# Optimization experiments

Measured on AMD Instinct MI355X. Metric: run time of the kernel, lower is better.

The kernel has to match this reference:

```python
import jax, jax.numpy as jnp
import numpy as np

HEADS = 8
EPS = 1e-6

def _feature_map(x):
    return jax.nn.elu(x) + 1.0

def _linear_attention(q, k, v, motion_weight):
    # q,k,v: [..., N, dh]; motion_weight broadcastable to q or None
    q = _feature_map(q)
    k = _feature_map(k)
    if motion_weight is not None:
        q = q * motion_weight
    k_sum = k.sum(axis=-2, keepdims=True)                      # [...,1,dh]
    kv = jnp.einsum('...nd,...ne->...de', k, v)                # [...,dh,dh]
    out = jnp.einsum('...nd,...de->...ne', q, kv)              # [...,N,dh]
    z = 1.0 / (jnp.einsum('...nd,...md->...nm', q, k_sum) + EPS)  # [...,N,1]
    return out * z

def setup_inputs() -> dict:
    key = jax.random.key(0)
    k1, k2, k3, k4 = jax.random.split(key, 4)
    B, T, H, W, C = 2, 16, 48, 48, 512
    x = jax.random.normal(k1, (B, T, H, W, C), dtype=jnp.float32)
    motion_mag = jax.random.normal(k2, (B, T, H, W, 1), dtype=jnp.float32)
    W_qkv = jax.random.normal(k3, (C, 3 * C), dtype=jnp.float32) * 0.02
    temporal_emb = jax.random.normal(k4, (1, 1, 1, 1, C), dtype=jnp.float32)
    return {"x": x, "motion_mag": motion_mag, "W_qkv": W_qkv, "temporal_emb": temporal_emb}

def _split_heads(t, lead, n, heads, dh):
    # t: [lead, n, heads*dh] -> [lead, heads, n, dh]
    return t.reshape(lead, n, heads, dh).transpose(0, 2, 1, 3)

def reference(x, motion_mag, W_qkv, temporal_emb):
    B, T, H, W, C = x.shape
    dh = C // HEADS
    x = x + temporal_emb

    # ---- temporal linear attention over frame-averaged tokens ----
    x_time = x.reshape(B, T, H * W, C).mean(axis=2)            # [B,T,C]
    qkv = x_time @ W_qkv                                       # [B,T,3C]
    q, k, v = jnp.split(qkv, 3, axis=-1)
    q = _split_heads(q, B, T, HEADS, dh)                       # [B,h,T,dh]
    k = _split_heads(k, B, T, HEADS, dh)
    v = _split_heads(v, B, T, HEADS, dh)
    mm = motion_mag.reshape(B, T, -1).mean(axis=-1, keepdims=True)  # [B,T,1]
    mw_t = 1.0 + jnp.tanh(mm)[:, None]                         # [B,1,T,1]
    t_out = _linear_attention(q, k, v, mw_t)                   # [B,h,T,dh]
    t_out = t_out.transpose(0, 2, 1, 3).reshape(B, T, C)       # [B,T,C]

    # broadcast temporal output over spatial dims
    x_sp = x + t_out[:, :, None, None, :]                      # [B,T,H,W,C]

    # ---- global spatial linear attention per frame ----
    N = H * W
    x_flat = x_sp.reshape(B * T, N, C)
    qkv = x_flat @ W_qkv                                       # [BT,N,3C]
    q, k, v = jnp.split(qkv, 3, axis=-1)
    q = _split_heads(q, B * T, N, HEADS, dh)                   # [BT,h,N,dh]
    k = _split_heads(k, B * T, N, HEADS, dh)
    v = _split_heads(v, B * T, N, HEADS, dh)
    mm2 = motion_mag.reshape(B * T, N, 1)
    mw_s = 1.0 + jnp.tanh(mm2)[:, None]                        # [BT,1,N,1]
    s_out = _linear_attention(q, k, v, mw_s)                   # [BT,h,N,dh]
    s_out = s_out.transpose(0, 2, 1, 3).reshape(B, T, H, W, C)
    return s_out
```

## Files before the change

kernel.cpp:

```cpp
#include <hip/hip_runtime.h>
#include <cstddef>
#include <cstdint>

#define HEADS 8
#define DH 64
#define C 512
#define TC 1536
#define BT 32
#define NTOK 2304
#define TT 16
#define EPS 1e-6f

typedef __attribute__((ext_vector_type(8))) short bf16x8;
typedef __attribute__((ext_vector_type(4))) float f32x4;
typedef __attribute__((address_space(3))) void as3_void;
typedef __attribute__((address_space(1))) const void as1_cvoid;

__device__ __forceinline__ float fmap(float x) {
    return x > 0.f ? x + 1.f : __expf(x);
}
__device__ __forceinline__ unsigned short f2bf(float f) {
    unsigned int u = __float_as_uint(f);
    return (unsigned short)((u + 0x7fffu + ((u >> 16) & 1u)) >> 16);
}
__device__ __forceinline__ unsigned int pack2bf(float a, float b) {
    return (unsigned int)f2bf(a) | ((unsigned int)f2bf(b) << 16);
}
__device__ __forceinline__ float bf2f(unsigned short h) {
    return __uint_as_float(((unsigned int)h) << 16);
}
__device__ __forceinline__ void gload16(const void* g, void* l) {
    __builtin_amdgcn_global_load_lds((as1_cvoid*)(uintptr_t)g,
                                     (as3_void*)(uintptr_t)l, 16, 0, 0);
}

__global__ __launch_bounds__(256) void k_prep_w(
    const float* __restrict__ W, unsigned short* __restrict__ Wt) {
    __shared__ float tile[32][33];
    int col0 = blockIdx.x * 32, c0 = blockIdx.y * 32;
    int tx = threadIdx.x & 31, ty = threadIdx.x >> 5;
#pragma unroll
    for (int j = 0; j < 4; ++j) {
        int c = ty + j * 8;
        tile[c][tx] = W[(size_t)(c0 + c) * TC + col0 + tx];
    }
    __syncthreads();
#pragma unroll
    for (int j = 0; j < 4; ++j) {
        int col = ty + j * 8;
        Wt[(size_t)(col0 + col) * C + c0 + tx] = f2bf(tile[tx][col]);
    }
}

__global__ __launch_bounds__(256) void k_time_reduce(
    const float* __restrict__ x, const float* __restrict__ motion,
    float* __restrict__ xtraw, float* __restrict__ mmraw,
    unsigned short* __restrict__ xb) {
    int bt = blockIdx.x, sp = blockIdx.y, tid = threadIdx.x;
    int n0 = sp * 288, cid = tid * 2;
    const float* xp = x + ((size_t)(bt * NTOK + n0)) * C + cid;
    unsigned short* xbp = xb + ((size_t)(bt * NTOK + n0)) * C + cid;
    float s0 = 0.f, s1 = 0.f;
    for (int n = 0; n < 288; ++n) {
        float2 v = *(const float2*)(xp + (size_t)n * C);
        s0 += v.x;
        s1 += v.y;
        *(unsigned int*)(xbp + (size_t)n * C) = pack2bf(v.x, v.y);
    }
    atomicAdd(&xtraw[bt * C + cid], s0);
    atomicAdd(&xtraw[bt * C + cid + 1], s1);

    const float* mp = motion + (size_t)bt * NTOK + n0;
    float m = mp[tid];
    if (tid < 32) m += mp[256 + tid];
    __shared__ float red[256];
    red[tid] = m;
    __syncthreads();
    for (int s = 128; s > 0; s >>= 1) {
        if (tid < s) red[tid] += red[tid + s];
        __syncthreads();
    }
    if (tid == 0) atomicAdd(&mmraw[bt], red[0]);
}

__global__ __launch_bounds__(256) void k_time_qkv(
    const float* __restrict__ xtraw, const float* __restrict__ temb,
    const float* __restrict__ W, float* __restrict__ qkvt) {
    int bt = blockIdx.x, col = blockIdx.y * 256 + threadIdx.x, tid = threadIdx.x;
    __shared__ float xl[C];
    xl[tid]       = xtraw[bt * C + tid]       * (1.f / NTOK) + temb[tid];
    xl[tid + 256] = xtraw[bt * C + tid + 256] * (1.f / NTOK) + temb[tid + 256];
    __syncthreads();
    float a = 0.f;
#pragma unroll 8
    for (int c = 0; c < C; ++c) a += xl[c] * W[(size_t)c * TC + col];
    qkvt[(size_t)bt * TC + col] = a;
}

__global__ __launch_bounds__(256) void k_time_attn(
    const float* __restrict__ qkvt, const float* __restrict__ mmraw,
    const float* __restrict__ temb, float* __restrict__ bias) {
    int b = blockIdx.x, h = blockIdx.y, tid = threadIdx.x;
    int d = tid & 63, g = tid >> 6;
    __shared__ float qs[TT][DH], ks[TT][DH], vs[TT][DH], ksum[DH];
    __shared__ float kvl[DH][DH];
    for (int t = g; t < TT; t += 4) {
        size_t base = (size_t)(b * TT + t) * TC + h * DH + d;
        float mwt = 1.f + tanhf(mmraw[b * TT + t] * (1.f / NTOK));
        qs[t][d] = fmap(qkvt[base]) * mwt;
        ks[t][d] = fmap(qkvt[base + C]);
        vs[t][d] = qkvt[base + 2 * C];
    }
    __syncthreads();
    if (g == 0) {
        float s = 0.f;
        for (int t = 0; t < TT; ++t) s += ks[t][d];
        ksum[d] = s;
    }
    float kva[16];
#pragma unroll
    for (int i = 0; i < 16; ++i) kva[i] = 0.f;
    for (int t = 0; t < TT; ++t) {
        float kd = ks[t][d];
#pragma unroll
        for (int i = 0; i < 16; ++i) kva[i] += kd * vs[t][g * 16 + i];
    }
#pragma unroll
    for (int i = 0; i < 16; ++i) kvl[d][g * 16 + i] = kva[i];
    __syncthreads();
    for (int tt = 0; tt < 4; ++tt) {
        int t = g * 4 + tt;
        float acc = 0.f, zden = 0.f;
        for (int dd = 0; dd < DH; ++dd) {
            float qv = qs[t][dd];
            acc  += qv * kvl[dd][d];
            zden += qv * ksum[dd];
        }
        bias[(size_t)(b * TT + t) * C + h * DH + d] =
            acc / (zden + EPS) + temb[h * DH + d];
    }
}

__global__ __launch_bounds__(256) void k_bias_vec(
    const float* __restrict__ bias, const float* __restrict__ W,
    float* __restrict__ bvec) {
    int bt = blockIdx.x, col = blockIdx.y * 256 + threadIdx.x, tid = threadIdx.x;
    __shared__ float bl[C];
    bl[tid]       = bias[bt * C + tid];
    bl[tid + 256] = bias[bt * C + tid + 256];
    __syncthreads();
    float a = 0.f;
#pragma unroll 8
    for (int c = 0; c < C; ++c) a += bl[c] * W[(size_t)c * TC + col];
    bvec[(size_t)bt * TC + col] = a;
}

__global__ __launch_bounds__(512) void k_spatial_kv(
    const unsigned short* __restrict__ xb, const unsigned short* __restrict__ Wt,
    const float* __restrict__ bvec, float* __restrict__ kvw,
    float* __restrict__ ksw) {
    __shared__ __align__(16) char smem[99328];
    unsigned short* A0 = (unsigned short*)smem;
    unsigned short* B0 = (unsigned short*)(smem + 16384);
    unsigned short* A1 = (unsigned short*)(smem + 49152);
    unsigned short* B1 = (unsigned short*)(smem + 65536);
    char* kvT = smem + 16384;
    float* bvl = (float*)(smem + 98304);

    const int s = blockIdx.x, hp = blockIdx.y, bt = blockIdx.z;
    const int tid = threadIdx.x, lane = tid & 63, w = tid >> 6;
    const int lm = lane & 15, quad = lane >> 4;
    const int mr = w & 1, nc = w >> 1;
    const int li8 = lane >> 3, lp = lane & 7;

    if (tid < 256) {
        int h2 = tid >> 7, j2 = tid & 127;
        int wr = (j2 < 64) ? (C + (hp * 2 + h2) * DH + j2)
                           : (2 * C + (hp * 2 + h2) * DH + (j2 - 64));
        bvl[tid] = bvec[(size_t)bt * TC + wr];
    }
    const unsigned short* srcA[2];
#pragma unroll
    for (int l = 0; l < 2; ++l) {
        int row = w * 16 + l * 8 + li8;
        int c = lp ^ (row & 7);
        srcA[l] = xb + ((size_t)(bt * NTOK + row)) * C + c * 8;
    }
    const unsigned short* srcB[4];
#pragma unroll
    for (int l = 0; l < 4; ++l) {
        int r = w * 32 + l * 8 + li8;
        int c = lp ^ (r & 7);
        int h2 = r >> 7, j2 = r & 127;
        int wr = (j2 < 64) ? (C + (hp * 2 + h2) * DH + j2)
                           : (2 * C + (hp * 2 + h2) * DH + (j2 - 64));
        srcB[l] = Wt + (size_t)wr * C + c * 8;
    }

    float ksp0 = 0.f, ksp1 = 0.f;
    f32x4 kvacc[2][2];
#pragma unroll
    for (int a = 0; a < 2; ++a)
#pragma unroll
        for (int b = 0; b < 2; ++b) kvacc[a][b] = (f32x4)0.f;

    auto STAGE = [&](unsigned short* As, unsigned short* Bs, int n0, int kc) {
#pragma unroll
        for (int l = 0; l < 2; ++l)
            gload16(srcA[l] + (size_t)n0 * C + kc * 64, As + (w * 16 + l * 8) * 64);
#pragma unroll
        for (int l = 0; l < 4; ++l)
            gload16(srcB[l] + kc * 64, Bs + (w * 32 + l * 8) * 64);
    };

#pragma unroll 1
    for (int t = 0; t < 3; ++t) {
        const int n0 = (s * 3 + t) * 128;
        f32x4 acc[4][4];
#pragma unroll
        for (int i = 0; i < 4; ++i)
#pragma unroll
            for (int j = 0; j < 4; ++j) acc[i][j] = (f32x4)0.f;

        STAGE(A0, B0, n0, 0);
        __syncthreads();
#pragma unroll
        for (int kc = 0; kc < 8; ++kc) {
            const unsigned short* As = (kc & 1) ? A1 : A0;
            const unsigned short* Bs = (kc & 1) ? B1 : B0;
            if (kc < 7) {
                STAGE((kc & 1) ? A0 : A1, (kc & 1) ? B0 : B1, n0, kc + 1);
                __builtin_amdgcn_sched_barrier(0);
            }
#pragma unroll
            for (int ks = 0; ks < 2; ++ks) {
                bf16x8 af[4], bfr[4];
#pragma unroll
                for (int i = 0; i < 4; ++i) {
                    int row = mr * 64 + i * 16 + lm;
                    int p = (ks * 4 + quad) ^ (row & 7);
                    af[i] = *(const bf16x8*)&As[row * 64 + p * 8];
                }
#pragma unroll
                for (int j = 0; j < 4; ++j) {
                    int row = nc * 64 + j * 16 + lm;
                    int p = (ks * 4 + quad) ^ (row & 7);
                    bfr[j] = *(const bf16x8*)&Bs[row * 64 + p * 8];
                }
#pragma unroll
                for (int i = 0; i < 4; ++i)
#pragma unroll
                    for (int j = 0; j < 4; ++j)
                        acc[i][j] = __builtin_amdgcn_mfma_f32_16x16x32_bf16(
                            af[i], bfr[j], acc[i][j], 0, 0, 0);
            }
            __syncthreads();
        }
#pragma unroll 1
        for (int ph = 0; ph < 2; ++ph) {
            __syncthreads();
            if ((nc >> 1) == ph) {
#pragma unroll
                for (int i = 0; i < 4; ++i) {
                    int tokb = mr * 64 + i * 16 + quad * 4;
                    int tc = tokb >> 3;
#pragma unroll
                    for (int j = 0; j < 4; ++j) {
                        int cg = nc * 64 + j * 16 + lm;
                        int cl = cg & 127;
                        float bv = bvl[cg];
                        f32x4 a4 = acc[i][j];
                        float v0 = a4[0] + bv, v1 = a4[1] + bv;
                        float v2 = a4[2] + bv, v3 = a4[3] + bv;
                        if (cl < 64) {
                            v0 = fmap(v0); v1 = fmap(v1);
                            v2 = fmap(v2); v3 = fmap(v3);
                        }
                        int p = (tc & 8) | ((tc & 7) ^ (cl & 7));
                        uint2 pk;
                        pk.x = pack2bf(v0, v1);
                        pk.y = pack2bf(v2, v3);
                        *(uint2*)(kvT + cl * 256 + p * 16 + (tokb & 7) * 2) = pk;
                    }
                }
            }
            __syncthreads();
            if (tid < 128) {
                int d = tid & 63, half = tid >> 6;
                float ssum = 0.f;
#pragma unroll
                for (int tc2 = 0; tc2 < 8; ++tc2) {
                    int tcc = half * 8 + tc2;
                    int p = (tcc & 8) | ((tcc & 7) ^ (d & 7));
                    bf16x8 v8 = *(const bf16x8*)(kvT + d * 256 + p * 16);
#pragma unroll
                    for (int q = 0; q < 8; ++q)
                        ssum += bf2f((unsigned short)v8[q]);
                }
                if (ph == 0) ksp0 += ssum; else ksp1 += ssum;
            }
#pragma unroll
            for (int dt2 = 0; dt2 < 2; ++dt2) {
                int drow = (mr * 2 + dt2) * 16 + lm;
                int erow = 64 + nc * 16 + lm;
#pragma unroll
                for (int ks2 = 0; ks2 < 4; ++ks2) {
                    int tcc = ks2 * 4 + quad;
                    int pA = (tcc & 8) | ((tcc & 7) ^ (drow & 7));
                    int pB = (tcc & 8) | ((tcc & 7) ^ (erow & 7));
                    bf16x8 ak = *(const bf16x8*)(kvT + drow * 256 + pA * 16);
                    bf16x8 bv8 = *(const bf16x8*)(kvT + erow * 256 + pB * 16);
                    kvacc[ph][dt2] = __builtin_amdgcn_mfma_f32_16x16x32_bf16(
                        ak, bv8, kvacc[ph][dt2], 0, 0, 0);
                }
            }
        }
        __syncthreads();
    }
#pragma unroll
    for (int ph = 0; ph < 2; ++ph) {
        float* kvp = kvw + (size_t)(bt * HEADS + hp * 2 + ph) * DH * DH;
#pragma unroll
        for (int dt2 = 0; dt2 < 2; ++dt2) {
            int d0 = (mr * 2 + dt2) * 16 + quad * 4;
            int e = nc * 16 + lm;
#pragma unroll
            for (int r = 0; r < 4; ++r)
                atomicAdd(&kvp[(d0 + r) * DH + e], kvacc[ph][dt2][r]);
        }
    }
    if (tid < 128) {
        int d = tid & 63;
        atomicAdd(&ksw[(bt * HEADS + hp * 2 + 0) * DH + d], ksp0);
        atomicAdd(&ksw[(bt * HEADS + hp * 2 + 1) * DH + d], ksp1);
    }
}

__global__ __launch_bounds__(256) void k_spatial_out(
    const unsigned short* __restrict__ xb, const unsigned short* __restrict__ Wt,
    const float* __restrict__ bvec, const float* __restrict__ motion,
    const float* __restrict__ kvw, const float* __restrict__ ksw,
    float* __restrict__ out) {
    __shared__ __align__(16) char smem[51712];
    unsigned short* A_s = (unsigned short*)smem;
    unsigned short* B_s = (unsigned short*)(smem + 16384);
    char* qs  = smem;
    char* kvT = smem + 32768;
    float* bvl = (float*)(smem + 49152);
    float* mwv = (float*)(smem + 49664);
    float* ksl = (float*)(smem + 50176);
    float* zv  = (float*)(smem + 50688);

    const int tile = blockIdx.x, hp = blockIdx.y, bt = blockIdx.z;
    const int tid = threadIdx.x, lane = tid & 63, w = tid >> 6;
    const int lm = lane & 15, quad = lane >> 4;
    const int mr = w & 1, nc = w >> 1;
    const int li8 = lane >> 3, lp = lane & 7;
    const int n0 = tile * 128;

    if (tid < 128) {
        bvl[tid] = bvec[(size_t)bt * TC + hp * 128 + tid];
        mwv[tid] = 1.f + tanhf(motion[(size_t)bt * NTOK + n0 + tid]);
        ksl[tid] = ksw[(bt * HEADS + hp * 2 + (tid >> 6)) * DH + (tid & 63)];
    }
    {
        int rr = tid & 127, hh = tid >> 7;
        int head = rr >> 6, e = rr & 63;
        const float* kvp = kvw + (size_t)(bt * HEADS + hp * 2 + head) * DH * DH;
#pragma unroll 8
        for (int d = hh * 32; d < hh * 32 + 32; ++d) {
            int p = (d >> 3) ^ (rr & 7);
            ((unsigned short*)(kvT + rr * 128 + p * 16))[d & 7] = f2bf(kvp[d * DH + e]);
        }
    }
    f32x4 acc[4][4];
#pragma unroll
    for (int i = 0; i < 4; ++i)
#pragma unroll
        for (int j = 0; j < 4; ++j) acc[i][j] = (f32x4)0.f;

    for (int kc = 0; kc < 8; ++kc) {
        __syncthreads();
#pragma unroll
        for (int l = 0; l < 4; ++l) {
            int rowbase = w * 32 + l * 8;
            int row = rowbase + li8;
            int c = lp ^ (row & 7);
            gload16(xb + ((size_t)(bt * NTOK + n0 + row)) * C + kc * 64 + c * 8,
                    A_s + rowbase * 64);
        }
#pragma unroll
        for (int l = 0; l < 4; ++l) {
            int rowbase = w * 32 + l * 8;
            int r = rowbase + li8;
            int c = lp ^ (r & 7);
            gload16(Wt + (size_t)(hp * 128 + r) * C + kc * 64 + c * 8,
                    B_s + rowbase * 64);
        }
        __syncthreads();
#pragma unroll
        for (int ks = 0; ks < 2; ++ks) {
            bf16x8 af[4], bfr[4];
#pragma unroll
            for (int i = 0; i < 4; ++i) {
                int row = mr * 64 + i * 16 + lm;
                int p = (ks * 4 + quad) ^ (row & 7);
                af[i] = *(const bf16x8*)&A_s[row * 64 + p * 8];
            }
#pragma unroll
            for (int j = 0; j < 4; ++j) {
                int row = nc * 64 + j * 16 + lm;
                int p = (ks * 4 + quad) ^ (row & 7);
                bfr[j] = *(const bf16x8*)&B_s[row * 64 + p * 8];
            }
#pragma unroll
            for (int i = 0; i < 4; ++i)
#pragma unroll
                for (int j = 0; j < 4; ++j)
                    acc[i][j] = __builtin_amdgcn_mfma_f32_16x16x32_bf16(
                        af[i], bfr[j], acc[i][j], 0, 0, 0);
        }
    }
    __syncthreads();
#pragma unroll
    for (int i = 0; i < 4; ++i) {
#pragma unroll
        for (int j = 0; j < 4; ++j) {
            int cl = nc * 64 + j * 16 + lm;
            float bv = bvl[cl];
            int cch = cl >> 3;
#pragma unroll
            for (int r = 0; r < 4; ++r) {
                int tok = mr * 64 + i * 16 + quad * 4 + r;
                float qv = fmap(acc[i][j][r] + bv) * mwv[tok];
                int p = (cch & 8) | ((cch & 7) ^ (tok & 7));
                ((unsigned short*)(qs + tok * 256 + p * 16))[cl & 7] = f2bf(qv);
            }
        }
    }
    __syncthreads();
    {
        int head = tid >> 7, tok = tid & 127;
        float zd = 0.f;
#pragma unroll
        for (int tc3 = 0; tc3 < 8; ++tc3) {
            int cch = head * 8 + tc3;
            int p = (cch & 8) | ((cch & 7) ^ (tok & 7));
            bf16x8 q8 = *(const bf16x8*)(qs + tok * 256 + p * 16);
#pragma unroll
            for (int q = 0; q < 8; ++q)
                zd += bf2f((unsigned short)q8[q]) * ksl[head * 64 + tc3 * 8 + q];
        }
        zv[head * 128 + tok] = 1.f / (zd + EPS);
    }
    __syncthreads();
    f32x4 oacc[4][4];
#pragma unroll
    for (int i = 0; i < 4; ++i)
#pragma unroll
        for (int j = 0; j < 4; ++j) oacc[i][j] = (f32x4)0.f;
#pragma unroll
    for (int ks3 = 0; ks3 < 2; ++ks3) {
        bf16x8 aq[4], bk[4];
#pragma unroll
        for (int i = 0; i < 4; ++i) {
            int tok = mr * 64 + i * 16 + lm;
            int cch = nc * 8 + ks3 * 4 + quad;
            int p = (cch & 8) | ((cch & 7) ^ (tok & 7));
            aq[i] = *(const bf16x8*)(qs + tok * 256 + p * 16);
        }
#pragma unroll
        for (int j = 0; j < 4; ++j) {
            int row = nc * 64 + j * 16 + lm;
            int tcc = ks3 * 4 + quad;
            int p = tcc ^ (row & 7);
            bk[j] = *(const bf16x8*)(kvT + row * 128 + p * 16);
        }
#pragma unroll
        for (int i = 0; i < 4; ++i)
#pragma unroll
            for (int j = 0; j < 4; ++j)
                oacc[i][j] = __builtin_amdgcn_mfma_f32_16x16x32_bf16(
                    aq[i], bk[j], oacc[i][j], 0, 0, 0);
    }
    const int h = hp * 2 + nc;
#pragma unroll
    for (int i = 0; i < 4; ++i)
#pragma unroll
        for (int r = 0; r < 4; ++r) {
            int tok = mr * 64 + i * 16 + quad * 4 + r;
            float z = zv[nc * 128 + tok];
#pragma unroll
            for (int j = 0; j < 4; ++j)
                out[((size_t)(bt * NTOK + n0 + tok)) * C + h * DH + j * 16 + lm] =
                    oacc[i][j][r] * z;
        }
}

extern "C" void kernel_launch(void* const* d_in, const int* in_sizes, int n_in,
                              void* d_out, int out_size, void* d_ws, size_t ws_size,
                              hipStream_t stream) {
    (void)in_sizes; (void)n_in; (void)out_size; (void)ws_size;
    const float* x      = (const float*)d_in[0];
    const float* motion = (const float*)d_in[1];
    const float* W      = (const float*)d_in[2];
    const float* temb   = (const float*)d_in[3];
    float* out = (float*)d_out;
    float* ws  = (float*)d_ws;

    float* kvw   = ws;
    float* ksw   = kvw + 1048576;
    float* xtraw = ksw + 16384;
    float* mmraw = xtraw + 16384;
    float* qkvt  = mmraw + 32;
    float* bias  = qkvt + 49152;
    float* bvec  = bias + 16384;
    unsigned short* Wt = (unsigned short*)(bvec + 49152);
    unsigned short* xb = (unsigned short*)(Wt + (size_t)TC * C);

    hipMemsetAsync(d_ws, 0,
                   (size_t)(1048576 + 16384 + 16384 + 32) * sizeof(float), stream);
    k_prep_w<<<dim3(48, 16), 256, 0, stream>>>(W, Wt);
    k_time_reduce<<<dim3(BT, 8), 256, 0, stream>>>(x, motion, xtraw, mmraw, xb);
    k_time_qkv<<<dim3(BT, 6), 256, 0, stream>>>(xtraw, temb, W, qkvt);
    k_time_attn<<<dim3(2, HEADS), 256, 0, stream>>>(qkvt, mmraw, temb, bias);
    k_bias_vec<<<dim3(BT, 6), 256, 0, stream>>>(bias, W, bvec);
    k_spatial_kv<<<dim3(6, 4, BT), 512, 0, stream>>>(xb, Wt, bvec, kvw, ksw);
    k_spatial_out<<<dim3(18, 4, BT), 256, 0, stream>>>(xb, Wt, bvec, motion,
                                                       kvw, ksw, out);
}
```

Measured before the change: 539.5 us.

## Triple-buffer A tiles with explicit vmcnt waits in spatial KV GEMM

```diff
diff --git a/kernel.cpp b/kernel.cpp
--- a/kernel.cpp
+++ b/kernel.cpp
@@ -15,6 +15,9 @@
 typedef __attribute__((ext_vector_type(4))) float f32x4;
 typedef __attribute__((address_space(3))) void as3_void;
 typedef __attribute__((address_space(1))) const void as1_cvoid;
+
+#define SBAR() __builtin_amdgcn_s_barrier()
+#define SCHED0() __builtin_amdgcn_sched_barrier(0)
 
 __device__ __forceinline__ float fmap(float x) {
     return x > 0.f ? x + 1.f : __expf(x);
@@ -159,13 +162,16 @@
     const unsigned short* __restrict__ xb, const unsigned short* __restrict__ Wt,
     const float* __restrict__ bvec, float* __restrict__ kvw,
     float* __restrict__ ksw) {
-    __shared__ __align__(16) char smem[99328];
-    unsigned short* A0 = (unsigned short*)smem;
-    unsigned short* B0 = (unsigned short*)(smem + 16384);
-    unsigned short* A1 = (unsigned short*)(smem + 49152);
-    unsigned short* B1 = (unsigned short*)(smem + 65536);
-    char* kvT = smem + 16384;
-    float* bvl = (float*)(smem + 98304);
+    __shared__ __align__(16) char smem[115712];
+    unsigned short* const Abuf[3] = {
+        (unsigned short*)smem,
+        (unsigned short*)(smem + 16384),
+        (unsigned short*)(smem + 32768)};
+    unsigned short* const Bbuf[2] = {
+        (unsigned short*)(smem + 49152),
+        (unsigned short*)(smem + 81920)};
+    char* kvT = smem + 49152;
+    float* bvl = (float*)(smem + 114688);
 
     const int s = blockIdx.x, hp = blockIdx.y, bt = blockIdx.z;
     const int tid = threadIdx.x, lane = tid & 63, w = tid >> 6;
@@ -204,10 +210,12 @@
 #pragma unroll
         for (int b = 0; b < 2; ++b) kvacc[a][b] = (f32x4)0.f;
 
-    auto STAGE = [&](unsigned short* As, unsigned short* Bs, int n0, int kc) {
+    auto STAGE_A = [&](unsigned short* As, int n0, int kc) {
 #pragma unroll
         for (int l = 0; l < 2; ++l)
             gload16(srcA[l] + (size_t)n0 * C + kc * 64, As + (w * 16 + l * 8) * 64);
+    };
+    auto STAGE_B = [&](unsigned short* Bs, int kc) {
 #pragma unroll
         for (int l = 0; l < 4; ++l)
             gload16(srcB[l] + kc * 64, Bs + (w * 32 + l * 8) * 64);
@@ -222,16 +230,32 @@
 #pragma unroll
             for (int j = 0; j < 4; ++j) acc[i][j] = (f32x4)0.f;
 
-        STAGE(A0, B0, n0, 0);
-        __syncthreads();
+        STAGE_A(Abuf[0], n0, 0);
+        STAGE_B(Bbuf[0], 0);
+        SCHED0();
+        STAGE_A(Abuf[1], n0, 1);
+        SCHED0();
 #pragma unroll
         for (int kc = 0; kc < 8; ++kc) {
-            const unsigned short* As = (kc & 1) ? A1 : A0;
-            const unsigned short* Bs = (kc & 1) ? B1 : B0;
+            const unsigned short* As = Abuf[kc % 3];
+            const unsigned short* Bs = Bbuf[kc & 1];
             if (kc < 7) {
-                STAGE((kc & 1) ? A0 : A1, (kc & 1) ? B0 : B1, n0, kc + 1);
-                __builtin_amdgcn_sched_barrier(0);
-            }
+                STAGE_B(Bbuf[(kc + 1) & 1], kc + 1);
+                SCHED0();
+            }
+            if (kc < 6) {
+                STAGE_A(Abuf[(kc + 2) % 3], n0, kc + 2);
+                SCHED0();
+            }
+            if (kc < 6)
+                asm volatile("s_waitcnt vmcnt(8)" ::: "memory");
+            else if (kc == 6)
+                asm volatile("s_waitcnt vmcnt(6)" ::: "memory");
+            else
+                asm volatile("s_waitcnt vmcnt(0)" ::: "memory");
+            SBAR();
+            SCHED0();
+            __builtin_amdgcn_s_setprio(1);
 #pragma unroll
             for (int ks = 0; ks < 2; ++ks) {
                 bf16x8 af[4], bfr[4];
@@ -254,7 +278,10 @@
                         acc[i][j] = __builtin_amdgcn_mfma_f32_16x16x32_bf16(
                             af[i], bfr[j], acc[i][j], 0, 0, 0);
             }
-            __syncthreads();
+            __builtin_amdgcn_s_setprio(0);
+            SCHED0();
+            SBAR();
+            SCHED0();
         }
 #pragma unroll 1
         for (int ph = 0; ph < 2; ++ph) {
```

Measured after the change: 531.9 us. Within noise of the previous version (-1.4%).

## Split spatial KV kernel to one head per block with 256 threads

Applied to the files above, without the earlier changes.

```diff
diff --git a/kernel.cpp b/kernel.cpp
--- a/kernel.cpp
+++ b/kernel.cpp
@@ -15,6 +15,8 @@
 typedef __attribute__((ext_vector_type(4))) float f32x4;
 typedef __attribute__((address_space(3))) void as3_void;
 typedef __attribute__((address_space(1))) const void as1_cvoid;
+
+#define SCHED0() __builtin_amdgcn_sched_barrier(0)
 
 __device__ __forceinline__ float fmap(float x) {
     return x > 0.f ? x + 1.f : __expf(x);
@@ -155,34 +157,35 @@
     bvec[(size_t)bt * TC + col] = a;
 }
 
-__global__ __launch_bounds__(512) void k_spatial_kv(
+__global__ __launch_bounds__(256) void k_spatial_kv(
     const unsigned short* __restrict__ xb, const unsigned short* __restrict__ Wt,
     const float* __restrict__ bvec, float* __restrict__ kvw,
     float* __restrict__ ksw) {
-    __shared__ __align__(16) char smem[99328];
-    unsigned short* A0 = (unsigned short*)smem;
-    unsigned short* B0 = (unsigned short*)(smem + 16384);
-    unsigned short* A1 = (unsigned short*)(smem + 49152);
-    unsigned short* B1 = (unsigned short*)(smem + 65536);
-    char* kvT = smem + 16384;
-    float* bvl = (float*)(smem + 98304);
-
-    const int s = blockIdx.x, hp = blockIdx.y, bt = blockIdx.z;
+    __shared__ __align__(16) char smem[66048];
+    unsigned short* const Abuf[2] = {
+        (unsigned short*)smem,
+        (unsigned short*)(smem + 16384)};
+    unsigned short* const Bbuf[2] = {
+        (unsigned short*)(smem + 32768),
+        (unsigned short*)(smem + 49152)};
+    char* kvT = smem + 32768;
+    float* bvl = (float*)(smem + 65536);
+
+    const int s = blockIdx.x, h = blockIdx.y, bt = blockIdx.z;
     const int tid = threadIdx.x, lane = tid & 63, w = tid >> 6;
     const int lm = lane & 15, quad = lane >> 4;
     const int mr = w & 1, nc = w >> 1;
     const int li8 = lane >> 3, lp = lane & 7;
 
-    if (tid < 256) {
-        int h2 = tid >> 7, j2 = tid & 127;
-        int wr = (j2 < 64) ? (C + (hp * 2 + h2) * DH + j2)
-                           : (2 * C + (hp * 2 + h2) * DH + (j2 - 64));
+    if (tid < 128) {
+        int cl = tid;
+        int wr = (cl < 64) ? (C + h * DH + cl) : (2 * C + h * DH + (cl - 64));
         bvl[tid] = bvec[(size_t)bt * TC + wr];
     }
-    const unsigned short* srcA[2];
-#pragma unroll
-    for (int l = 0; l < 2; ++l) {
-        int row = w * 16 + l * 8 + li8;
+    const unsigned short* srcA[4];
+#pragma unroll
+    for (int l = 0; l < 4; ++l) {
+        int row = w * 32 + l * 8 + li8;
         int c = lp ^ (row & 7);
         srcA[l] = xb + ((size_t)(bt * NTOK + row)) * C + c * 8;
     }
@@ -191,26 +194,25 @@
     for (int l = 0; l < 4; ++l) {
         int r = w * 32 + l * 8 + li8;
         int c = lp ^ (r & 7);
-        int h2 = r >> 7, j2 = r & 127;
-        int wr = (j2 < 64) ? (C + (hp * 2 + h2) * DH + j2)
-                           : (2 * C + (hp * 2 + h2) * DH + (j2 - 64));
+        int wr = (r < 64) ? (C + h * DH + r) : (2 * C + h * DH + (r - 64));
         srcB[l] = Wt + (size_t)wr * C + c * 8;
     }
 
-    float ksp0 = 0.f, ksp1 = 0.f;
+    float ksp = 0.f;
     f32x4 kvacc[2][2];
 #pragma unroll
     for (int a = 0; a < 2; ++a)
 #pragma unroll
         for (int b = 0; b < 2; ++b) kvacc[a][b] = (f32x4)0.f;
 
-    auto STAGE = [&](unsigned short* As, unsigned short* Bs, int n0, int kc) {
-#pragma unroll
-        for (int l = 0; l < 2; ++l)
-            gload16(srcA[l] + (size_t)n0 * C + kc * 64, As + (w * 16 + l * 8) * 64);
+    auto STAGE = [&](int buf, int n0, int kc) {
 #pragma unroll
         for (int l = 0; l < 4; ++l)
-            gload16(srcB[l] + kc * 64, Bs + (w * 32 + l * 8) * 64);
+            gload16(srcA[l] + (size_t)n0 * C + kc * 64,
+                    Abuf[buf] + (w * 32 + l * 8) * 64);
+#pragma unroll
+        for (int l = 0; l < 4; ++l)
+            gload16(srcB[l] + kc * 64, Bbuf[buf] + (w * 32 + l * 8) * 64);
     };
 
 #pragma unroll 1
@@ -222,15 +224,15 @@
 #pragma unroll
             for (int j = 0; j < 4; ++j) acc[i][j] = (f32x4)0.f;
 
-        STAGE(A0, B0, n0, 0);
+        STAGE(0, n0, 0);
         __syncthreads();
 #pragma unroll
         for (int kc = 0; kc < 8; ++kc) {
-            const unsigned short* As = (kc & 1) ? A1 : A0;
-            const unsigned short* Bs = (kc & 1) ? B1 : B0;
+            const unsigned short* As = Abuf[kc & 1];
+            const unsigned short* Bs = Bbuf[kc & 1];
             if (kc < 7) {
-                STAGE((kc & 1) ? A0 : A1, (kc & 1) ? B0 : B1, n0, kc + 1);
-                __builtin_amdgcn_sched_barrier(0);
+                STAGE((kc + 1) & 1, n0, kc + 1);
+                SCHED0();
             }
 #pragma unroll
             for (int ks = 0; ks < 2; ++ks) {
@@ -256,53 +258,49 @@
             }
             __syncthreads();
         }
-#pragma unroll 1
-        for (int ph = 0; ph < 2; ++ph) {
-            __syncthreads();
-            if ((nc >> 1) == ph) {
-#pragma unroll
-                for (int i = 0; i < 4; ++i) {
-                    int tokb = mr * 64 + i * 16 + quad * 4;
-                    int tc = tokb >> 3;
-#pragma unroll
-                    for (int j = 0; j < 4; ++j) {
-                        int cg = nc * 64 + j * 16 + lm;
-                        int cl = cg & 127;
-                        float bv = bvl[cg];
-                        f32x4 a4 = acc[i][j];
-                        float v0 = a4[0] + bv, v1 = a4[1] + bv;
-                        float v2 = a4[2] + bv, v3 = a4[3] + bv;
-                        if (cl < 64) {
-                            v0 = fmap(v0); v1 = fmap(v1);
-                            v2 = fmap(v2); v3 = fmap(v3);
-                        }
-                        int p = (tc & 8) | ((tc & 7) ^ (cl & 7));
-                        uint2 pk;
-                        pk.x = pack2bf(v0, v1);
-                        pk.y = pack2bf(v2, v3);
-                        *(uint2*)(kvT + cl * 256 + p * 16 + (tokb & 7) * 2) = pk;
-                    }
+#pragma unroll
+        for (int i = 0; i < 4; ++i) {
+            int tokb = mr * 64 + i * 16 + quad * 4;
+            int tc = tokb >> 3;
+#pragma unroll
+            for (int j = 0; j < 4; ++j) {
+                int cl = nc * 64 + j * 16 + lm;
+                float bv = bvl[cl];
+                f32x4 a4 = acc[i][j];
+                float v0 = a4[0] + bv, v1 = a4[1] + bv;
+                float v2 = a4[2] + bv, v3 = a4[3] + bv;
+                if (cl < 64) {
+                    v0 = fmap(v0); v1 = fmap(v1);
+                    v2 = fmap(v2); v3 = fmap(v3);
                 }
-            }
-            __syncthreads();
-            if (tid < 128) {
-                int d = tid & 63, half = tid >> 6;
-                float ssum = 0.f;
-#pragma unroll
-                for (int tc2 = 0; tc2 < 8; ++tc2) {
-                    int tcc = half * 8 + tc2;
-                    int p = (tcc & 8) | ((tcc & 7) ^ (d & 7));
-                    bf16x8 v8 = *(const bf16x8*)(kvT + d * 256 + p * 16);
-#pragma unroll
-                    for (int q = 0; q < 8; ++q)
-                        ssum += bf2f((unsigned short)v8[q]);
-                }
-                if (ph == 0) ksp0 += ssum; else ksp1 += ssum;
-            }
+                int p = (tc & 8) | ((tc & 7) ^ (cl & 7));
+                uint2 pk;
+                pk.x = pack2bf(v0, v1);
+                pk.y = pack2bf(v2, v3);
+                *(uint2*)(kvT + cl * 256 + p * 16 + (tokb & 7) * 2) = pk;
+            }
+        }
+        __syncthreads();
+        if (tid < 128) {
+            int d = tid & 63, half = tid >> 6;
+            float ssum = 0.f;
+#pragma unroll
+            for (int tc2 = 0; tc2 < 8; ++tc2) {
+                int tcc = half * 8 + tc2;
+                int p = (tcc & 8) | ((tcc & 7) ^ (d & 7));
+                bf16x8 v8 = *(const bf16x8*)(kvT + d * 256 + p * 16);
+#pragma unroll
+                for (int q = 0; q < 8; ++q)
+                    ssum += bf2f((unsigned short)v8[q]);
+            }
+            ksp += ssum;
+        }
+#pragma unroll
+        for (int et2 = 0; et2 < 2; ++et2) {
 #pragma unroll
             for (int dt2 = 0; dt2 < 2; ++dt2) {
                 int drow = (mr * 2 + dt2) * 16 + lm;
-                int erow = 64 + nc * 16 + lm;
+                int erow = 64 + (nc * 2 + et2) * 16 + lm;
 #pragma unroll
                 for (int ks2 = 0; ks2 < 4; ++ks2) {
                     int tcc = ks2 * 4 + quad;
@@ -310,30 +308,27 @@
                     int pB = (tcc & 8) | ((tcc & 7) ^ (erow & 7));
                     bf16x8 ak = *(const bf16x8*)(kvT + drow * 256 + pA * 16);
                     bf16x8 bv8 = *(const bf16x8*)(kvT + erow * 256 + pB * 16);
-                    kvacc[ph][dt2] = __builtin_amdgcn_mfma_f32_16x16x32_bf16(
-                        ak, bv8, kvacc[ph][dt2], 0, 0, 0);
+                    kvacc[et2][dt2] = __builtin_amdgcn_mfma_f32_16x16x32_bf16(
+                        ak, bv8, kvacc[et2][dt2], 0, 0, 0);
                 }
             }
         }
         __syncthreads();
     }
-#pragma unroll
-    for (int ph = 0; ph < 2; ++ph) {
-        float* kvp = kvw + (size_t)(bt * HEADS + hp * 2 + ph) * DH * DH;
+    float* kvp = kvw + (size_t)(bt * HEADS + h) * DH * DH;
+#pragma unroll
+    for (int et2 = 0; et2 < 2; ++et2) {
 #pragma unroll
         for (int dt2 = 0; dt2 < 2; ++dt2) {
             int d0 = (mr * 2 + dt2) * 16 + quad * 4;
-            int e = nc * 16 + lm;
+            int e = (nc * 2 + et2) * 16 + lm;
 #pragma unroll
             for (int r = 0; r < 4; ++r)
-                atomicAdd(&kvp[(d0 + r) * DH + e], kvacc[ph][dt2][r]);
-        }
-    }
-    if (tid < 128) {
-        int d = tid & 63;
-        atomicAdd(&ksw[(bt * HEADS + hp * 2 + 0) * DH + d], ksp0);
-        atomicAdd(&ksw[(bt * HEADS + hp * 2 + 1) * DH + d], ksp1);
-    }
+                atomicAdd(&kvp[(d0 + r) * DH + e], kvacc[et2][dt2][r]);
+        }
+    }
+    if (tid < 128)
+        atomicAdd(&ksw[(bt * HEADS + h) * DH + (tid & 63)], ksp);
 }
 
 __global__ __launch_bounds__(256) void k_spatial_out(
@@ -525,7 +520,7 @@
     k_time_qkv<<<dim3(BT, 6), 256, 0, stream>>>(xtraw, temb, W, qkvt);
     k_time_attn<<<dim3(2, HEADS), 256, 0, stream>>>(qkvt, mmraw, temb, bias);
     k_bias_vec<<<dim3(BT, 6), 256, 0, stream>>>(bias, W, bvec);
-    k_spatial_kv<<<dim3(6, 4, BT), 512, 0, stream>>>(xb, Wt, bvec, kvw, ksw);
+    k_spatial_kv<<<dim3(6, HEADS, BT), 256, 0, stream>>>(xb, Wt, bvec, kvw, ksw);
     k_spatial_out<<<dim3(18, 4, BT), 256, 0, stream>>>(xb, Wt, bvec, motion,
                                                        kvw, ksw, out);
 }
```

Measured after the change: 550.4 us. +2.0%, slower.
